# Kernel tuning notes

Measured on AMD Instinct MI355X. Metric: run time of the kernel, lower is better.

## Reference

```python
import jax, jax.numpy as jnp
import numpy as np

B, T, S, F_IN, F_OUT, K, L = 8, 8, 500, 32, 64, 3, 3


def setup_inputs() -> dict:
    key = jax.random.key(0)
    ks = jax.random.split(key, 10)
    x = jax.random.normal(ks[0], (B, T, S, F_IN), dtype=jnp.float32)
    Adj_t = jax.random.uniform(ks[1], (T, T), dtype=jnp.float32)
    Adj_s = jax.random.uniform(ks[2], (S, S), dtype=jnp.float32)
    # small mixing coefficients so Adj^k stays numerically tame
    s = jax.random.uniform(ks[3], (4,), dtype=jnp.float32) * 0.005
    H = jax.random.normal(ks[4], (L, K, F_OUT, F_OUT), dtype=jnp.float32) / jnp.sqrt(F_OUT)
    W1 = jax.random.normal(ks[5], (F_OUT, F_IN), dtype=jnp.float32) / jnp.sqrt(F_IN)
    b1 = jax.random.normal(ks[6], (F_OUT,), dtype=jnp.float32) * 0.01
    W2 = jax.random.normal(ks[7], (F_OUT, F_OUT), dtype=jnp.float32) / jnp.sqrt(F_OUT)
    b2 = jax.random.normal(ks[8], (F_OUT,), dtype=jnp.float32) * 0.01
    merge = jax.random.normal(ks[9], (T,), dtype=jnp.float32)
    return {"x": x, "Adj_t": Adj_t, "Adj_s": Adj_s, "s": s, "H": H,
            "W1": W1, "b1": b1, "W2": W2, "b2": b2, "merge": merge}


def reference(x, Adj_t, Adj_s, s, H, W1, b1, W2, b2, merge):
    Bx, Tx, Sx, Fin = x.shape
    N = Tx * Sx
    n_layers, Kk = H.shape[0], H.shape[1]
    I_t = jnp.eye(Tx, dtype=x.dtype)
    I_s = jnp.eye(Sx, dtype=x.dtype)
    I_st = jnp.eye(N, dtype=x.dtype)
    # mixed Kronecker product-graph adjacency, (T*S) x (T*S)
    Adj = (s[0] * I_st
           + s[1] * jnp.kron(I_t, Adj_s)
           + s[2] * jnp.kron(Adj_t, I_s)
           + s[3] * jnp.kron(Adj_t, Adj_s))
    # cache Adj^k for k = 0..K-1 (same math as per-layer matrix_power)
    powers = [I_st]
    for _ in range(1, Kk):
        powers.append(powers[-1] @ Adj)
    xf = x.reshape(Bx, N, Fin) @ W1.T + b1  # [B, N, F_out]
    for l in range(n_layers):
        acc = jnp.zeros_like(xf)
        for k in range(Kk):
            acc = acc + jnp.einsum('nm,bmf->bnf', powers[k], xf) @ H[l, k]
        xf = jnp.tanh(acc)
    xf = xf @ W2.T + b2  # [B, N, F_out]
    xo = xf.reshape(Bx, Tx, Sx, -1)  # [B, T, S, F_out]
    # transpose(3,1) -> [B,F,S,T]; matmul(merge) contracts T; transpose(2,1) -> [B,S,F]
    return jnp.einsum('btsf,t->bsf', xo, merge)
```

## Files before the change

kernel.cpp:

```cpp
#include <hip/hip_runtime.h>

#define BB 8
#define TT 8
#define SS 500
#define SP 512
#define FIN 32
#define FF 64
#define NBT 64
#define KT 1536
#define LROW_S 136
#define HROW 200
#define WROW 196
#define OROW 520

typedef short bf16x8 __attribute__((ext_vector_type(8)));
typedef float floatx4 __attribute__((ext_vector_type(4)));

__device__ __forceinline__ unsigned f2bf(float x) {
    unsigned u = __builtin_bit_cast(unsigned, x);
    return (u + 0x7FFFu + ((u >> 16) & 1u)) >> 16;
}
__device__ __forceinline__ float bf2f(unsigned short h) {
    unsigned u = ((unsigned)h) << 16;
    return __builtin_bit_cast(float, u);
}
__device__ __forceinline__ float ftanh(float x) {
    float ax = fabsf(x);
    float e = __expf(-2.f * ax);
    float r = (1.f - e) * __builtin_amdgcn_rcpf(1.f + e);
    return copysignf(r, x);
}

__device__ __forceinline__ void ctab(int m, float s0, float s1, float s2, float s3,
                                     float& c0, float& c1, float& c2) {
    c0 = 0.f; c1 = 0.f; c2 = 0.f;
    switch (m) {
        case 0: c0 = 1.f; c1 = s0; c2 = s0 * s0; break;
        case 1: c1 = s1; c2 = 2.f * s0 * s1; break;
        case 2: c2 = s1 * s1; break;
        case 3: c1 = s2; c2 = 2.f * s0 * s2; break;
        case 4: c1 = s3; c2 = 2.f * (s0 * s3 + s1 * s2); break;
        case 5: c2 = 2.f * s1 * s3; break;
        case 6: c2 = s2 * s2; break;
        case 7: c2 = 2.f * s2 * s3; break;
        case 8: c2 = s3 * s3; break;
    }
}

__global__ __launch_bounds__(256) void setup_k(const float* __restrict__ x,
                                               const float* __restrict__ W1,
                                               const float* __restrict__ b1,
                                               const float* __restrict__ As,
                                               const float* __restrict__ At,
                                               const float* __restrict__ sc,
                                               const float* __restrict__ H,
                                               unsigned short* __restrict__ Asb,
                                               unsigned short* __restrict__ AsbT,
                                               unsigned short* __restrict__ HcT,
                                               float* __restrict__ CtT,
                                               unsigned short* __restrict__ xfT,
                                               unsigned short* __restrict__ Abig0) {
    int tid = threadIdx.x;
    if (blockIdx.x < 512) {
        __shared__ float Xs[64][FIN + 1];
        __shared__ float Wl[FIN][FF];
        __shared__ float Ot[64][FF + 1];
        __shared__ float bl[FF];
        int bt = blockIdx.x >> 3, s0 = (blockIdx.x & 7) * 64;
        int b = bt >> 3, t = bt & 7;

        for (int i = tid; i < FIN * FF; i += 256) { int f = i >> 5, j = i & 31; Wl[j][f] = W1[i]; }
        if (tid < FF) bl[tid] = b1[tid];
        const float* xb = x + (size_t)bt * SS * FIN;
        #pragma unroll
        for (int i = 0; i < 8; ++i) {
            int lin = i * 256 + tid; int r = lin >> 5, j = lin & 31;
            int s = s0 + r;
            Xs[r][j] = (s < SS) ? xb[(size_t)s * FIN + j] : 0.f;
        }
        __syncthreads();
        int f = tid & 63, sq = tid >> 6;
        for (int i = 0; i < 16; ++i) {
            int r = sq * 16 + i;
            float acc = bl[f];
            #pragma unroll
            for (int j = 0; j < FIN; ++j) acc += Xs[r][j] * Wl[j][f];
            Ot[r][f] = (s0 + r < SS) ? acc : 0.f;
        }
        __syncthreads();
        #pragma unroll
        for (int it = 0; it < 2; ++it) {
            int idx = it * 256 + tid;
            int row = idx >> 3, c = idx & 7;
            int4 w;
            unsigned short tmp[8];
            #pragma unroll
            for (int q = 0; q < 8; ++q) tmp[q] = (unsigned short)f2bf(Ot[row][c * 8 + q]);
            w.x = tmp[0] | (tmp[1] << 16); w.y = tmp[2] | (tmp[3] << 16);
            w.z = tmp[4] | (tmp[5] << 16); w.w = tmp[6] | (tmp[7] << 16);
            *(int4*)(Abig0 + (size_t)(b * SP + s0 + row) * KT + t * 192 + c * 8) = w;
        }
        {
            int ff = tid >> 2, scol = (tid & 3) * 16;
            unsigned short tmp[16];
            #pragma unroll
            for (int i = 0; i < 16; ++i) tmp[i] = (unsigned short)f2bf(Ot[scol + i][ff]);
            unsigned short* dp = xfT + ((size_t)bt * FF + ff) * SP + s0 + scol;
            #pragma unroll
            for (int q = 0; q < 2; ++q) {
                int4 w;
                w.x = tmp[q*8+0] | (tmp[q*8+1] << 16); w.y = tmp[q*8+2] | (tmp[q*8+3] << 16);
                w.z = tmp[q*8+4] | (tmp[q*8+5] << 16); w.w = tmp[q*8+6] | (tmp[q*8+7] << 16);
                *(int4*)(dp + q * 8) = w;
            }
        }
        return;
    }
    int idx = (blockIdx.x - 512) * 256 + tid;
    if (idx < 262144) {
        int s = idx >> 9, k = idx & 511;
        Asb[idx] = (s < SS && k < SS) ? (unsigned short)f2bf(As[(size_t)s * SS + k]) : 0;
    } else if (idx < 524288) {
        int r = idx - 262144;
        int j = r >> 9, k = r & 511;
        AsbT[r] = (j < SS && k < SS) ? (unsigned short)f2bf(As[(size_t)k * SS + j]) : 0;
    } else {
        int r = idx - 524288;
        if (r < 110592) {
            int l = r / 36864;
            int r2 = r - l * 36864;
            int row = r2 / 192;
            int col = r2 - row * 192;
            int p = row >> 6, f = row & 63;
            int bp = col >> 6, j = col & 63;
            float s0 = sc[0], s1 = sc[1], s2 = sc[2], s3 = sc[3];
            float c0, c1, c2;
            ctab(p * 3 + bp, s0, s1, s2, s3, c0, c1, c2);
            float val = c0 * H[((size_t)(l * 3 + 0) * 64 + j) * 64 + f]
                      + c1 * H[((size_t)(l * 3 + 1) * 64 + j) * 64 + f]
                      + c2 * H[((size_t)(l * 3 + 2) * 64 + j) * 64 + f];
            HcT[r] = (unsigned short)f2bf(val);
        } else if (r < 110784) {
            int i2 = r - 110592;
            int pt = i2 >> 3, t = i2 & 7;
            int p = pt >> 3, tp = pt & 7;
            float val;
            if (p == 0) val = (t == tp) ? 1.f : 0.f;
            else if (p == 1) val = At[t * 8 + tp];
            else {
                val = 0.f;
                #pragma unroll
                for (int kk = 0; kk < 8; ++kk) val += At[t * 8 + kk] * At[kk * 8 + tp];
            }
            CtT[i2] = val;
        }
    }
}

__global__ __launch_bounds__(256) void prep2_k(const unsigned short* __restrict__ Asb,
                                               const unsigned short* __restrict__ AsbT,
                                               unsigned short* __restrict__ Asqb) {
    int tid = threadIdx.x;
    int wave = tid >> 6, lane = tid & 63;
    int l16 = lane & 15, quad = lane >> 4;
    int st = blockIdx.x, ct = blockIdx.y;

    const unsigned short* ap = Asb + (size_t)(st * 16 + l16) * SP + quad * 8;
    const unsigned short* bp = AsbT + (size_t)(ct * 64 + wave * 16 + l16) * SP + quad * 8;
    floatx4 acc = {};
    #pragma unroll 4
    for (int k0 = 0; k0 < SP; k0 += 32)
        acc = __builtin_amdgcn_mfma_f32_16x16x32_bf16(*(const bf16x8*)(ap + k0),
                                                      *(const bf16x8*)(bp + k0), acc, 0, 0, 0);
    int j = ct * 64 + wave * 16 + l16;
    int i0 = st * 16 + quad * 4;
    #pragma unroll
    for (int r = 0; r < 4; ++r)
        Asqb[(size_t)(i0 + r) * SP + j] = (unsigned short)f2bf(acc[r]);
}

__global__ __launch_bounds__(256) void smm_k(const unsigned short* __restrict__ Asb,
                                             const unsigned short* __restrict__ Asqb,
                                             const unsigned short* __restrict__ xfT,
                                             unsigned short* __restrict__ Abig) {
    __shared__ unsigned short A1[64 * LROW_S];
    __shared__ unsigned short A2[64 * LROW_S];
    __shared__ unsigned short Bt[64 * LROW_S];

    int tid = threadIdx.x;
    int wave = tid >> 6, lane = tid & 63;
    int l16 = lane & 15, quad = lane >> 4;
    int m0 = blockIdx.x * 64, bt = blockIdx.y;
    int b = bt >> 3, t = bt & 7;

    const unsigned short* a1g = Asb + (size_t)m0 * SP;
    const unsigned short* a2g = Asqb + (size_t)m0 * SP;
    const unsigned short* bg  = xfT + (size_t)bt * FF * SP;

    floatx4 acc1[4] = {}, acc2[4] = {};

    for (int k0 = 0; k0 < SP; k0 += 128) {
        __syncthreads();
        #pragma unroll
        for (int it = 0; it < 4; ++it) {
            int idx = it * 256 + tid;
            int row = idx >> 4, c = idx & 15;
            int4 v1 = *(const int4*)(a1g + (size_t)row * SP + k0 + c * 8);
            int4 v2 = *(const int4*)(a2g + (size_t)row * SP + k0 + c * 8);
            int4 vb = *(const int4*)(bg  + (size_t)row * SP + k0 + c * 8);
            *(int4*)&A1[row * LROW_S + c * 8] = v1;
            *(int4*)&A2[row * LROW_S + c * 8] = v2;
            *(int4*)&Bt[row * LROW_S + c * 8] = vb;
        }
        __syncthreads();
        #pragma unroll
        for (int ks = 0; ks < 4; ++ks) {
            bf16x8 af1 = *(const bf16x8*)&A1[(wave * 16 + l16) * LROW_S + ks * 32 + quad * 8];
            bf16x8 af2 = *(const bf16x8*)&A2[(wave * 16 + l16) * LROW_S + ks * 32 + quad * 8];
            #pragma unroll
            for (int nt = 0; nt < 4; ++nt) {
                bf16x8 bf = *(const bf16x8*)&Bt[(nt * 16 + l16) * LROW_S + ks * 32 + quad * 8];
                acc1[nt] = __builtin_amdgcn_mfma_f32_16x16x32_bf16(af1, bf, acc1[nt], 0, 0, 0);
                acc2[nt] = __builtin_amdgcn_mfma_f32_16x16x32_bf16(af2, bf, acc2[nt], 0, 0, 0);
            }
        }
    }

    __syncthreads();
    #pragma unroll
    for (int nt = 0; nt < 4; ++nt)
        #pragma unroll
        for (int r = 0; r < 4; ++r) {
            A1[(wave * 16 + quad * 4 + r) * LROW_S + nt * 16 + l16] = (unsigned short)f2bf(acc1[nt][r]);
            A2[(wave * 16 + quad * 4 + r) * LROW_S + nt * 16 + l16] = (unsigned short)f2bf(acc2[nt][r]);
        }
    __syncthreads();
    int row = wave * 16 + (lane >> 2);
    int c2 = (lane & 3) * 2;
    #pragma unroll
    for (int q = 0; q < 2; ++q) {
        int c = c2 + q;
        int4 v1 = *(const int4*)&A1[row * LROW_S + c * 8];
        int4 v2 = *(const int4*)&A2[row * LROW_S + c * 8];
        size_t base = (size_t)(b * SP + m0 + row) * KT + t * 192;
        *(int4*)(Abig + base + 64 + c * 8)  = v1;
        *(int4*)(Abig + base + 128 + c * 8) = v2;
    }
}

__global__ __launch_bounds__(256) void hmix_k(const unsigned short* __restrict__ Abig,
                                              const unsigned short* __restrict__ HcT_l,
                                              const float* __restrict__ CtT,
                                              const float* __restrict__ W2,
                                              const float* __restrict__ b2,
                                              const float* __restrict__ merge,
                                              unsigned short* __restrict__ xfT_out,
                                              unsigned short* __restrict__ Abig_out,
                                              float* __restrict__ out,
                                              int wflag) {
    __shared__ char smem[76800];
    __shared__ float CtS[192];
    __shared__ float mlS[8];
    unsigned short* Bs  = (unsigned short*)smem;
    float* Wl           = (float*)smem;
    unsigned short* Ob  = (unsigned short*)(smem + 50176);
    float* W2l          = (float*)(smem + 50176);
    float* zt           = (float*)(smem + 66816);

    int tid = threadIdx.x;
    int wave = tid >> 6, lane = tid & 63;
    int l16 = lane & 15, quad = lane >> 4;
    int wm = wave & 1, wn = wave >> 1;
    int s0 = blockIdx.x * 8, b = blockIdx.y;

    if (tid < 192) CtS[tid] = CtT[tid];
    if (tid < 8) mlS[tid] = merge[tid];

    bf16x8 afr[2][6];
    {
        const unsigned short* abase =
            Abig + (size_t)(b * SP + s0 + (l16 & 7)) * KT + quad * 8;
        #pragma unroll
        for (int mt = 0; mt < 2; ++mt) {
            int tp = (wm * 2 + mt) * 2 + (l16 >> 3);
            #pragma unroll
            for (int ks = 0; ks < 6; ++ks)
                afr[mt][ks] = *(const bf16x8*)(abase + tp * 192 + ks * 32);
        }
    }

    {
        int br = tid >> 3, bc = tid & 7;
        #pragma unroll
        for (int it = 0; it < 6; ++it) {
            int row = it * 32 + br;
            const unsigned short* hp = HcT_l + (size_t)row * 192;
            #pragma unroll
            for (int j = 0; j < 3; ++j) {
                int c = bc + j * 8;
                *(int4*)&Bs[row * HROW + c * 8] = *(const int4*)(hp + c * 8);
            }
        }
    }
    __syncthreads();

    floatx4 acc[2][6] = {};
    #pragma unroll
    for (int ks = 0; ks < 6; ++ks) {
        bf16x8 bfr[6];
        #pragma unroll
        for (int nt = 0; nt < 6; ++nt)
            bfr[nt] = *(const bf16x8*)&Bs[((wn * 6 + nt) * 16 + l16) * HROW + ks * 32 + quad * 8];
        #pragma unroll
        for (int mt = 0; mt < 2; ++mt)
            #pragma unroll
            for (int nt = 0; nt < 6; ++nt)
                acc[mt][nt] = __builtin_amdgcn_mfma_f32_16x16x32_bf16(afr[mt][ks], bfr[nt], acc[mt][nt], 0, 0, 0);
    }

    __syncthreads();

    #pragma unroll
    for (int mt = 0; mt < 2; ++mt)
        #pragma unroll
        for (int nt = 0; nt < 6; ++nt) {
            int col = (wn * 6 + nt) * 16 + l16;
            #pragma unroll
            for (int r = 0; r < 4; ++r) {
                int fr = quad * 4 + r;
                int tp = (wm * 2 + mt) * 2 + (fr >> 3);
                int srow = fr & 7;
                Wl[(tp * 8 + srow) * WROW + col] = acc[mt][nt][r];
            }
        }
    if (!wflag) {
        for (int i = tid; i < 4096; i += 256) { int f = i >> 6, j = i & 63; W2l[j * 65 + f] = W2[i]; }
    }
    __syncthreads();

    int f = tid & 63, sg = tid >> 6;
    float th[8][2];
    {
        float o[8][2] = {};
        #pragma unroll
        for (int pt = 0; pt < 24; ++pt) {
            int tp = pt & 7, p = pt >> 3;
            float w0 = Wl[(tp * 8 + sg * 2 + 0) * WROW + p * 64 + f];
            float w1 = Wl[(tp * 8 + sg * 2 + 1) * WROW + p * 64 + f];
            #pragma unroll
            for (int t = 0; t < 8; ++t) {
                float cv = CtS[pt * 8 + t];
                o[t][0] += cv * w0;
                o[t][1] += cv * w1;
            }
        }
        #pragma unroll
        for (int t = 0; t < 8; ++t) {
            th[t][0] = ftanh(o[t][0]);
            th[t][1] = ftanh(o[t][1]);
        }
    }

    if (wflag) {
        #pragma unroll
        for (int t = 0; t < 8; ++t) {
            Ob[(sg * 2 + 0) * OROW + t * 64 + f] = (unsigned short)f2bf(th[t][0]);
            Ob[(sg * 2 + 1) * OROW + t * 64 + f] = (unsigned short)f2bf(th[t][1]);
        }
        __syncthreads();
        #pragma unroll
        for (int it = 0; it < 2; ++it) {
            int idx = it * 256 + tid;
            int row = idx >> 6, c = idx & 63;
            int t = c >> 3, c8 = c & 7;
            int4 v = *(const int4*)&Ob[row * OROW + c * 8];
            *(int4*)(Abig_out + (size_t)(b * SP + s0 + row) * KT + t * 192 + c8 * 8) = v;
        }
        #pragma unroll
        for (int it = 0; it < 2; ++it) {
            int u = it * 256 + tid;
            int t = u >> 6, ff = u & 63;
            unsigned short tmp[8];
            #pragma unroll
            for (int sl = 0; sl < 8; ++sl) tmp[sl] = Ob[sl * OROW + t * 64 + ff];
            int4 w;
            w.x = tmp[0] | (tmp[1] << 16); w.y = tmp[2] | (tmp[3] << 16);
            w.z = tmp[4] | (tmp[5] << 16); w.w = tmp[6] | (tmp[7] << 16);
            *(int4*)(xfT_out + ((size_t)(b * 8 + t) * FF + ff) * SP + s0) = w;
        }
    } else {
        float z0 = 0.f, z1 = 0.f;
        #pragma unroll
        for (int t = 0; t < 8; ++t) {
            z0 += mlS[t] * th[t][0];
            z1 += mlS[t] * th[t][1];
        }
        zt[(sg * 2 + 0) * 65 + f] = z0;
        zt[(sg * 2 + 1) * 65 + f] = z1;
        __syncthreads();
        float msum = 0.f;
        #pragma unroll
        for (int t = 0; t < 8; ++t) msum += mlS[t];
        float bv = b2[f] * msum;
        #pragma unroll
        for (int r = 0; r < 2; ++r) {
            int s = s0 + sg * 2 + r;
            if (s < SS) {
                float accv = bv;
                #pragma unroll
                for (int j = 0; j < FF; ++j) accv += zt[(sg * 2 + r) * 65 + j] * W2l[j * 65 + f];
                out[((size_t)b * SS + s) * FF + f] = accv;
            }
        }
    }
}

extern "C" void kernel_launch(void* const* d_in, const int* in_sizes, int n_in,
                              void* d_out, int out_size, void* d_ws, size_t ws_size,
                              hipStream_t stream) {
    const float* x     = (const float*)d_in[0];
    const float* At    = (const float*)d_in[1];
    const float* As    = (const float*)d_in[2];
    const float* sc    = (const float*)d_in[3];
    const float* H     = (const float*)d_in[4];
    const float* W1    = (const float*)d_in[5];
    const float* b1    = (const float*)d_in[6];
    const float* W2    = (const float*)d_in[7];
    const float* b2    = (const float*)d_in[8];
    const float* merge = (const float*)d_in[9];
    float* out = (float*)d_out;

    char* ws = (char*)d_ws;
    unsigned short* Asb   = (unsigned short*)(ws + 0);
    unsigned short* AsbT  = (unsigned short*)(ws + 524288);
    unsigned short* Asqb  = (unsigned short*)(ws + 1048576);
    unsigned short* HcT   = (unsigned short*)(ws + 1572864);
    float*          CtT   = (float*)(ws + 1794048);
    unsigned short* xfT0  = (unsigned short*)(ws + 6291456);
    unsigned short* xfT1  = (unsigned short*)(ws + 10485760);
    unsigned short* Abig0 = (unsigned short*)(ws + 14680064);
    unsigned short* Abig1 = (unsigned short*)(ws + 27262976);

    setup_k<<<2993, 256, 0, stream>>>(x, W1, b1, As, At, sc, H,
                                      Asb, AsbT, HcT, CtT, xfT0, Abig0);
    prep2_k<<<dim3(32, 8), 256, 0, stream>>>(Asb, AsbT, Asqb);

    unsigned short* xfT_cur = xfT0;  unsigned short* xfT_nxt = xfT1;
    unsigned short* Abig_cur = Abig0; unsigned short* Abig_nxt = Abig1;
    for (int l = 0; l < 3; ++l) {
        smm_k<<<dim3(8, NBT), 256, 0, stream>>>(Asb, Asqb, xfT_cur, Abig_cur);
        hmix_k<<<dim3(64, 8), 256, 0, stream>>>(Abig_cur,
                                                HcT + (size_t)l * 36864, CtT,
                                                W2, b2, merge,
                                                xfT_nxt, Abig_nxt, out,
                                                (l < 2) ? 1 : 0);
        unsigned short* tt = xfT_cur;  xfT_cur = xfT_nxt;  xfT_nxt = tt;
        unsigned short* tb = Abig_cur; Abig_cur = Abig_nxt; Abig_nxt = tb;
    }
}
```

Baseline: 159.3 us.

## Drop LDS staging in smm and hmix kernels, load MFMA fragments directly from global

The spatial-matmul kernel no longer stages A1/A2/xfT tiles through shared memory with barriers. Each wave now loads its MFMA fragments straight from global/L2, swaps operand roles so the outputs land as packed bf16 pairs written directly to Abig, and removes the LDS transpose epilogue. The hmix kernel likewise reads H fragments from global instead of copying them to LDS, which removes a barrier and shrinks shared-memory use enough to possibly raise occupancy. The cost is redundant global loads across waves and strided fragment loads that depend on cache hits.

```diff
diff --git a/kernel.cpp b/kernel.cpp
--- a/kernel.cpp
+++ b/kernel.cpp
@@ -8,7 +8,6 @@
 #define FF 64
 #define NBT 64
 #define KT 1536
-#define LROW_S 136
 #define HROW 200
 #define WROW 196
 #define OROW 520
@@ -183,68 +182,40 @@
                                              const unsigned short* __restrict__ Asqb,
                                              const unsigned short* __restrict__ xfT,
                                              unsigned short* __restrict__ Abig) {
-    __shared__ unsigned short A1[64 * LROW_S];
-    __shared__ unsigned short A2[64 * LROW_S];
-    __shared__ unsigned short Bt[64 * LROW_S];
-
     int tid = threadIdx.x;
     int wave = tid >> 6, lane = tid & 63;
     int l16 = lane & 15, quad = lane >> 4;
-    int m0 = blockIdx.x * 64, bt = blockIdx.y;
+    int bx = blockIdx.x, bt = blockIdx.y;
     int b = bt >> 3, t = bt & 7;
-
-    const unsigned short* a1g = Asb + (size_t)m0 * SP;
-    const unsigned short* a2g = Asqb + (size_t)m0 * SP;
-    const unsigned short* bg  = xfT + (size_t)bt * FF * SP;
-
-    floatx4 acc1[4] = {}, acc2[4] = {};
-
-    for (int k0 = 0; k0 < SP; k0 += 128) {
-        __syncthreads();
-        #pragma unroll
-        for (int it = 0; it < 4; ++it) {
-            int idx = it * 256 + tid;
-            int row = idx >> 4, c = idx & 15;
-            int4 v1 = *(const int4*)(a1g + (size_t)row * SP + k0 + c * 8);
-            int4 v2 = *(const int4*)(a2g + (size_t)row * SP + k0 + c * 8);
-            int4 vb = *(const int4*)(bg  + (size_t)row * SP + k0 + c * 8);
-            *(int4*)&A1[row * LROW_S + c * 8] = v1;
-            *(int4*)&A2[row * LROW_S + c * 8] = v2;
-            *(int4*)&Bt[row * LROW_S + c * 8] = vb;
-        }
-        __syncthreads();
-        #pragma unroll
-        for (int ks = 0; ks < 4; ++ks) {
-            bf16x8 af1 = *(const bf16x8*)&A1[(wave * 16 + l16) * LROW_S + ks * 32 + quad * 8];
-            bf16x8 af2 = *(const bf16x8*)&A2[(wave * 16 + l16) * LROW_S + ks * 32 + quad * 8];
-            #pragma unroll
-            for (int nt = 0; nt < 4; ++nt) {
-                bf16x8 bf = *(const bf16x8*)&Bt[(nt * 16 + l16) * LROW_S + ks * 32 + quad * 8];
-                acc1[nt] = __builtin_amdgcn_mfma_f32_16x16x32_bf16(af1, bf, acc1[nt], 0, 0, 0);
-                acc2[nt] = __builtin_amdgcn_mfma_f32_16x16x32_bf16(af2, bf, acc2[nt], 0, 0, 0);
-            }
-        }
-    }
-
-    __syncthreads();
+    int srow = bx * 64 + wave * 16 + l16;
+
+    const unsigned short* b1p = Asb  + (size_t)srow * SP + quad * 8;
+    const unsigned short* b2p = Asqb + (size_t)srow * SP + quad * 8;
+    const unsigned short* xp  = xfT + ((size_t)bt * FF + l16) * SP + quad * 8;
+
+    floatx4 acc[4][2] = {};
+    #pragma unroll 4
+    for (int k0 = 0; k0 < SP; k0 += 32) {
+        bf16x8 bf1 = *(const bf16x8*)(b1p + k0);
+        bf16x8 bf2 = *(const bf16x8*)(b2p + k0);
+        #pragma unroll
+        for (int ft = 0; ft < 4; ++ft) {
+            bf16x8 af = *(const bf16x8*)(xp + (size_t)(ft * 16) * SP + k0);
+            acc[ft][0] = __builtin_amdgcn_mfma_f32_16x16x32_bf16(af, bf1, acc[ft][0], 0, 0, 0);
+            acc[ft][1] = __builtin_amdgcn_mfma_f32_16x16x32_bf16(af, bf2, acc[ft][1], 0, 0, 0);
+        }
+    }
+
+    unsigned short* op = Abig + (size_t)(b * SP + srow) * KT + t * 192;
     #pragma unroll
-    for (int nt = 0; nt < 4; ++nt)
-        #pragma unroll
-        for (int r = 0; r < 4; ++r) {
-            A1[(wave * 16 + quad * 4 + r) * LROW_S + nt * 16 + l16] = (unsigned short)f2bf(acc1[nt][r]);
-            A2[(wave * 16 + quad * 4 + r) * LROW_S + nt * 16 + l16] = (unsigned short)f2bf(acc2[nt][r]);
-        }
-    __syncthreads();
-    int row = wave * 16 + (lane >> 2);
-    int c2 = (lane & 3) * 2;
-    #pragma unroll
-    for (int q = 0; q < 2; ++q) {
-        int c = c2 + q;
-        int4 v1 = *(const int4*)&A1[row * LROW_S + c * 8];
-        int4 v2 = *(const int4*)&A2[row * LROW_S + c * 8];
-        size_t base = (size_t)(b * SP + m0 + row) * KT + t * 192;
-        *(int4*)(Abig + base + 64 + c * 8)  = v1;
-        *(int4*)(Abig + base + 128 + c * 8) = v2;
+    for (int ft = 0; ft < 4; ++ft) {
+        #pragma unroll
+        for (int m = 0; m < 2; ++m) {
+            int2 w;
+            w.x = (int)(f2bf(acc[ft][m][0]) | (f2bf(acc[ft][m][1]) << 16));
+            w.y = (int)(f2bf(acc[ft][m][2]) | (f2bf(acc[ft][m][3]) << 16));
+            *(int2*)(op + (m ? 128 : 64) + ft * 16 + quad * 4) = w;
+        }
     }
 }
 
@@ -258,14 +229,13 @@
                                               unsigned short* __restrict__ Abig_out,
                                               float* __restrict__ out,
                                               int wflag) {
-    __shared__ char smem[76800];
+    __shared__ float Wl[64 * WROW];
+    __shared__ char smem2[18720];
     __shared__ float CtS[192];
     __shared__ float mlS[8];
-    unsigned short* Bs  = (unsigned short*)smem;
-    float* Wl           = (float*)smem;
-    unsigned short* Ob  = (unsigned short*)(smem + 50176);
-    float* W2l          = (float*)(smem + 50176);
-    float* zt           = (float*)(smem + 66816);
+    unsigned short* Ob = (unsigned short*)smem2;
+    float* W2l = (float*)smem2;
+    float* zt  = (float*)(smem2 + 16640);
 
     int tid = threadIdx.x;
     int wave = tid >> 6, lane = tid & 63;
@@ -289,36 +259,20 @@
         }
     }
 
-    {
-        int br = tid >> 3, bc = tid & 7;
-        #pragma unroll
-        for (int it = 0; it < 6; ++it) {
-            int row = it * 32 + br;
-            const unsigned short* hp = HcT_l + (size_t)row * 192;
-            #pragma unroll
-            for (int j = 0; j < 3; ++j) {
-                int c = bc + j * 8;
-                *(int4*)&Bs[row * HROW + c * 8] = *(const int4*)(hp + c * 8);
-            }
-        }
-    }
-    __syncthreads();
-
     floatx4 acc[2][6] = {};
+    const unsigned short* hb = HcT_l + (size_t)(wn * 6 * 16 + l16) * 192 + quad * 8;
     #pragma unroll
     for (int ks = 0; ks < 6; ++ks) {
         bf16x8 bfr[6];
         #pragma unroll
         for (int nt = 0; nt < 6; ++nt)
-            bfr[nt] = *(const bf16x8*)&Bs[((wn * 6 + nt) * 16 + l16) * HROW + ks * 32 + quad * 8];
+            bfr[nt] = *(const bf16x8*)(hb + (size_t)(nt * 16) * 192 + ks * 32);
         #pragma unroll
         for (int mt = 0; mt < 2; ++mt)
             #pragma unroll
             for (int nt = 0; nt < 6; ++nt)
                 acc[mt][nt] = __builtin_amdgcn_mfma_f32_16x16x32_bf16(afr[mt][ks], bfr[nt], acc[mt][nt], 0, 0, 0);
     }
-
-    __syncthreads();
 
     #pragma unroll
     for (int mt = 0; mt < 2; ++mt)
```

Measured after the change: 222.1 us. 39.5% more time.
